# Optimization experiments

Measured on AMD Instinct MI355X. Metric: run time of the kernel, lower is better.

The kernel has to match this reference:

```python
import jax, jax.numpy as jnp
import numpy as np

B, S, IN, OUT, E, K = 4, 4096, 1024, 1024, 8, 2
SCALE = 512.0  # alpha / r = 512 / 1
TEMP = 1.0


def setup_inputs() -> dict:
    key = jax.random.key(0)
    k1, k2, k3, k4 = jax.random.split(key, 4)
    return {
        "x": jax.random.normal(k1, (B, S, IN), dtype=jnp.float32),
        "lora_A": jax.random.normal(k2, (E, 1, IN), dtype=jnp.float32) * 0.02,
        "lora_B": jax.random.normal(k3, (E, OUT, 1), dtype=jnp.float32) * 0.02,
        "gate_w": jax.random.normal(k4, (E, IN), dtype=jnp.float32) * 0.02,
        "gate_b": jnp.zeros((E,), dtype=jnp.float32),
    }


def reference(x, lora_A, lora_B, gate_w, gate_b):
    # segment-level gating: mean over seq, softmax over experts
    seg = x.mean(axis=1)                                    # [B, IN]
    logits = (seg @ gate_w.T + gate_b) / TEMP               # [B, E]
    gate_scores = jax.nn.softmax(logits, axis=-1)           # [B, E]
    topk_scores, topk_idx = jax.lax.top_k(gate_scores, K)   # [B, K] (same for all tokens in segment)

    # dense all-expert LoRA compute (eval mode: dropout is identity)
    h = jnp.einsum('bsi,eri->bser', x, lora_A)              # [B, S, E, r]
    expert_outputs = jnp.einsum('bser,eor->bseo', h, lora_B) * SCALE  # [B, S, E, OUT]

    # gather top-k experts per segment (broadcast over seq) and weighted-sum
    sel = jnp.take_along_axis(expert_outputs, topk_idx[:, None, :, None], axis=2)  # [B, S, K, OUT]
    out = jnp.sum(sel * topk_scores[:, None, :, None], axis=2)  # [B, S, OUT]
    return out
```

## Files before the change

kernel.cpp:

```cpp
#include <hip/hip_runtime.h>

#define SCALE_F 512.0f

#define WS_H     0
#define WS_GPART 131072
#define WS_SELC  147456

__global__ __launch_bounds__(256) void k1_h_gate(
    const float* __restrict__ x, const float* __restrict__ lora_A,
    const float* __restrict__ gate_w, float* __restrict__ h,
    float* __restrict__ gpart)
{
    const int tid  = threadIdx.x;
    const int w    = tid >> 6;
    const int lane = tid & 63;
    const int tok0 = blockIdx.x * 8;

    __shared__ float xbuf[8 * 1024];

    float4 W[4][4];
#pragma unroll
    for (int rr = 0; rr < 4; ++rr) {
        const int row = 4 * w + rr;
        const float* rp = (row < 8) ? (lora_A + row * 1024)
                                    : (gate_w + (row - 8) * 1024);
        const float4* rp4 = (const float4*)rp;
#pragma unroll
        for (int j = 0; j < 4; ++j) W[rr][j] = rp4[lane + 64 * j];
    }

    const float4* src = (const float4*)(x + (size_t)tok0 * 1024);
    float4* dst = (float4*)xbuf;
#pragma unroll
    for (int j = 0; j < 8; ++j) dst[tid + 256 * j] = src[tid + 256 * j];
    __syncthreads();

    float gacc0 = 0.f, gacc1 = 0.f, gacc2 = 0.f, gacc3 = 0.f;

#pragma unroll 2
    for (int t = 0; t < 8; ++t) {
        const float4* xr = (const float4*)(xbuf + t * 1024);
        const float4 xv0 = xr[lane];
        const float4 xv1 = xr[lane + 64];
        const float4 xv2 = xr[lane + 128];
        const float4 xv3 = xr[lane + 192];

        float p[4];
#pragma unroll
        for (int rr = 0; rr < 4; ++rr) {
            const float4 a0 = W[rr][0], a1 = W[rr][1];
            const float4 a2 = W[rr][2], a3 = W[rr][3];
            float s;
            s  = xv0.x * a0.x + xv0.y * a0.y + xv0.z * a0.z + xv0.w * a0.w;
            s += xv1.x * a1.x + xv1.y * a1.y + xv1.z * a1.z + xv1.w * a1.w;
            s += xv2.x * a2.x + xv2.y * a2.y + xv2.z * a2.z + xv2.w * a2.w;
            s += xv3.x * a3.x + xv3.y * a3.y + xv3.z * a3.z + xv3.w * a3.w;
            p[rr] = s;
        }
#pragma unroll
        for (int off = 32; off > 0; off >>= 1) {
            p[0] += __shfl_xor(p[0], off);
            p[1] += __shfl_xor(p[1], off);
            p[2] += __shfl_xor(p[2], off);
            p[3] += __shfl_xor(p[3], off);
        }
        const int tok = tok0 + t;
        if (w < 2) {
            if (lane == 0) {
                float4 hv = make_float4(p[0], p[1], p[2], p[3]);
                *(float4*)(h + (size_t)tok * 8 + w * 4) = hv;
            }
        } else {
            gacc0 += p[0]; gacc1 += p[1]; gacc2 += p[2]; gacc3 += p[3];
        }
    }

    if (w >= 2 && lane == 0) {
        float4 gv = make_float4(gacc0, gacc1, gacc2, gacc3);
        *(float4*)(gpart + (size_t)blockIdx.x * 8 + (w - 2) * 4) = gv;
    }
}

__global__ __launch_bounds__(256) void k2_gate(
    const float* __restrict__ gpart, const float* __restrict__ gate_b,
    int* __restrict__ sel, float* __restrict__ coef)
{
    const int tid  = threadIdx.x;
    const int j    = tid & 7;
    const int pair = tid >> 3;
    const int b    = pair >> 3;
    const int e    = pair & 7;

    __shared__ float s_red[32][8];
    __shared__ float s_logit[32];

    float acc = 0.f;
#pragma unroll 8
    for (int k = 0; k < 64; ++k) {
        acc += gpart[(size_t)(b * 512 + j * 64 + k) * 8 + e];
    }
    s_red[pair][j] = acc;
    __syncthreads();

    if (j == 0) {
        float s = 0.f;
#pragma unroll
        for (int q = 0; q < 8; ++q) s += s_red[pair][q];
        s_logit[pair] = s * (1.0f / 4096.0f) + gate_b[e];
    }
    __syncthreads();

    if (tid < 4) {
        float sc[8];
        float m = -1e30f;
#pragma unroll
        for (int q = 0; q < 8; ++q) { sc[q] = s_logit[tid * 8 + q]; m = fmaxf(m, sc[q]); }
        float sum = 0.f;
#pragma unroll
        for (int q = 0; q < 8; ++q) { sc[q] = __expf(sc[q] - m); sum += sc[q]; }
        const float inv = 1.0f / sum;

        int i0 = 0;
#pragma unroll
        for (int q = 1; q < 8; ++q) if (sc[q] > sc[i0]) i0 = q;
        int i1 = (i0 == 0) ? 1 : 0;
#pragma unroll
        for (int q = 0; q < 8; ++q) if (q != i0 && sc[q] > sc[i1]) i1 = q;

        sel[tid * 2]      = i0;
        sel[tid * 2 + 1]  = i1;
        coef[tid * 2]     = SCALE_F * sc[i0] * inv;
        coef[tid * 2 + 1] = SCALE_F * sc[i1] * inv;
    }
}

__global__ __launch_bounds__(256) void k3_combine(
    const float* __restrict__ h, const int* __restrict__ sel,
    const float* __restrict__ coef, const float* __restrict__ lora_B,
    float* __restrict__ out)
{
    const int tid = threadIdx.x;
    const int blk = blockIdx.x;
    const int b   = blk >> 9;

    const int   i0 = sel[b * 2];
    const int   i1 = sel[b * 2 + 1];
    const float c0 = coef[b * 2];
    const float c1 = coef[b * 2 + 1];

    const float4 b0 = ((const float4*)(lora_B + i0 * 1024))[tid];
    const float4 b1 = ((const float4*)(lora_B + i1 * 1024))[tid];
    const float4 v0 = make_float4(c0 * b0.x, c0 * b0.y, c0 * b0.z, c0 * b0.w);
    const float4 v1 = make_float4(c1 * b1.x, c1 * b1.y, c1 * b1.z, c1 * b1.w);

    const int tok0 = blk * 8;
    float4* out4 = (float4*)out;
#pragma unroll
    for (int t = 0; t < 8; ++t) {
        const int tok = tok0 + t;
        const float h0 = h[tok * 8 + i0];
        const float h1 = h[tok * 8 + i1];
        float4 r;
        r.x = h0 * v0.x + h1 * v1.x;
        r.y = h0 * v0.y + h1 * v1.y;
        r.z = h0 * v0.z + h1 * v1.z;
        r.w = h0 * v0.w + h1 * v1.w;
        out4[(size_t)tok * 256 + tid] = r;
    }
}

extern "C" void kernel_launch(void* const* d_in, const int* in_sizes, int n_in,
                              void* d_out, int out_size, void* d_ws, size_t ws_size,
                              hipStream_t stream) {
    const float* x      = (const float*)d_in[0];
    const float* lora_A = (const float*)d_in[1];
    const float* lora_B = (const float*)d_in[2];
    const float* gate_w = (const float*)d_in[3];
    const float* gate_b = (const float*)d_in[4];
    float* out = (float*)d_out;

    float* ws    = (float*)d_ws;
    float* h     = ws + WS_H;
    float* gpart = ws + WS_GPART;
    int*   sel   = (int*)(ws + WS_SELC);
    float* coef  = ws + WS_SELC + 8;

    k1_h_gate<<<2048, 256, 0, stream>>>(x, lora_A, gate_w, h, gpart);
    k2_gate<<<1, 256, 0, stream>>>(gpart, gate_b, sel, coef);
    k3_combine<<<2048, 256, 0, stream>>>(h, sel, coef, lora_B, out);
}
```

Baseline: 137.9 us.

## Fuse three kernels into one cooperative persistent kernel with grid sync

Replaces the three-launch pipeline (projection plus gate partials, gate softmax/top-k, combine) with a single cooperative kernel. It uses a persistent grid sized by occupancy and a grid-wide barrier between phases, and each block redoes the tiny gate reduction itself. This removes two kernel launches and the serial single-block gate kernel. In exchange it pays the cost of a grid sync, has every block re-read the gate partials, and runs fewer blocks than the original 2048. The three-kernel path is kept as a fallback if the cooperative launch fails.

```diff
diff --git a/kernel.cpp b/kernel.cpp
--- a/kernel.cpp
+++ b/kernel.cpp
@@ -1,10 +1,172 @@
 #include <hip/hip_runtime.h>
+#include <hip/hip_cooperative_groups.h>
+
+namespace cg = cooperative_groups;
 
 #define SCALE_F 512.0f
 
 #define WS_H     0
 #define WS_GPART 131072
 #define WS_SELC  147456
+
+__global__ __launch_bounds__(256) void fused_moe(
+    const float* __restrict__ x, const float* __restrict__ lora_A,
+    const float* __restrict__ lora_B, const float* __restrict__ gate_w,
+    const float* __restrict__ gate_b, float* __restrict__ out,
+    float* __restrict__ h, float* __restrict__ gpart)
+{
+    const int tid  = threadIdx.x;
+    const int w    = tid >> 6;
+    const int lane = tid & 63;
+    const int grid = gridDim.x;
+
+    __shared__ float  xbuf[8 * 1024];
+    __shared__ float4 s_gred[4][2];
+    __shared__ int    s_sel[4][2];
+    __shared__ float  s_coef[4][2];
+
+    float4 W[4][4];
+#pragma unroll
+    for (int rr = 0; rr < 4; ++rr) {
+        const int row = 4 * w + rr;
+        const float* rp = (row < 8) ? (lora_A + row * 1024)
+                                    : (gate_w + (row - 8) * 1024);
+        const float4* rp4 = (const float4*)rp;
+#pragma unroll
+        for (int j = 0; j < 4; ++j) W[rr][j] = rp4[lane + 64 * j];
+    }
+
+    for (int c = blockIdx.x; c < 2048; c += grid) {
+        const int tok0 = c * 8;
+        const float4* src = (const float4*)(x + (size_t)tok0 * 1024);
+        float4* dst = (float4*)xbuf;
+#pragma unroll
+        for (int j = 0; j < 8; ++j) dst[tid + 256 * j] = src[tid + 256 * j];
+        __syncthreads();
+
+        float g0 = 0.f, g1 = 0.f, g2 = 0.f, g3 = 0.f;
+
+#pragma unroll 2
+        for (int t = 0; t < 8; ++t) {
+            const float4* xr = (const float4*)(xbuf + t * 1024);
+            const float4 xv0 = xr[lane];
+            const float4 xv1 = xr[lane + 64];
+            const float4 xv2 = xr[lane + 128];
+            const float4 xv3 = xr[lane + 192];
+
+            float p[4];
+#pragma unroll
+            for (int rr = 0; rr < 4; ++rr) {
+                const float4 a0 = W[rr][0], a1 = W[rr][1];
+                const float4 a2 = W[rr][2], a3 = W[rr][3];
+                float s;
+                s  = xv0.x * a0.x + xv0.y * a0.y + xv0.z * a0.z + xv0.w * a0.w;
+                s += xv1.x * a1.x + xv1.y * a1.y + xv1.z * a1.z + xv1.w * a1.w;
+                s += xv2.x * a2.x + xv2.y * a2.y + xv2.z * a2.z + xv2.w * a2.w;
+                s += xv3.x * a3.x + xv3.y * a3.y + xv3.z * a3.z + xv3.w * a3.w;
+                p[rr] = s;
+            }
+#pragma unroll
+            for (int off = 32; off > 0; off >>= 1) {
+                p[0] += __shfl_xor(p[0], off);
+                p[1] += __shfl_xor(p[1], off);
+                p[2] += __shfl_xor(p[2], off);
+                p[3] += __shfl_xor(p[3], off);
+            }
+            if (w < 2) {
+                if (lane == 0) {
+                    *(float4*)(h + (size_t)(tok0 + t) * 8 + w * 4) =
+                        make_float4(p[0], p[1], p[2], p[3]);
+                }
+            } else {
+                g0 += p[0]; g1 += p[1]; g2 += p[2]; g3 += p[3];
+            }
+        }
+        if (w >= 2 && lane == 0) {
+            *(float4*)(gpart + (size_t)c * 8 + (w - 2) * 4) =
+                make_float4(g0, g1, g2, g3);
+        }
+        __syncthreads();
+    }
+
+    __threadfence();
+    cg::this_grid().sync();
+
+    {
+        const float4* gp4 = (const float4*)(gpart + (size_t)w * 4096);
+        float4 acc = make_float4(0.f, 0.f, 0.f, 0.f);
+#pragma unroll
+        for (int q = 0; q < 16; ++q) {
+            const float4 v = gp4[lane + 64 * q];
+            acc.x += v.x; acc.y += v.y; acc.z += v.z; acc.w += v.w;
+        }
+#pragma unroll
+        for (int off = 2; off <= 32; off <<= 1) {
+            acc.x += __shfl_xor(acc.x, off);
+            acc.y += __shfl_xor(acc.y, off);
+            acc.z += __shfl_xor(acc.z, off);
+            acc.w += __shfl_xor(acc.w, off);
+        }
+        if (lane < 2) s_gred[w][lane] = acc;
+    }
+    __syncthreads();
+
+    if (tid < 4) {
+        const float4 lo = s_gred[tid][0];
+        const float4 hi = s_gred[tid][1];
+        float l[8] = { lo.x, lo.y, lo.z, lo.w, hi.x, hi.y, hi.z, hi.w };
+#pragma unroll
+        for (int e = 0; e < 8; ++e) l[e] = l[e] * (1.0f / 4096.0f) + gate_b[e];
+        float m = l[0];
+#pragma unroll
+        for (int e = 1; e < 8; ++e) m = fmaxf(m, l[e]);
+        float sum = 0.f;
+#pragma unroll
+        for (int e = 0; e < 8; ++e) { l[e] = expf(l[e] - m); sum += l[e]; }
+        const float inv = 1.0f / sum;
+
+        int i0 = 0;
+#pragma unroll
+        for (int e = 1; e < 8; ++e) if (l[e] > l[i0]) i0 = e;
+        int i1 = (i0 == 0) ? 1 : 0;
+#pragma unroll
+        for (int e = 0; e < 8; ++e) if (e != i0 && l[e] > l[i1]) i1 = e;
+
+        s_sel[tid][0]  = i0;
+        s_sel[tid][1]  = i1;
+        s_coef[tid][0] = SCALE_F * l[i0] * inv;
+        s_coef[tid][1] = SCALE_F * l[i1] * inv;
+    }
+    __syncthreads();
+
+    for (int c = blockIdx.x; c < 2048; c += grid) {
+        const int bb = c >> 9;
+        const int   i0 = s_sel[bb][0];
+        const int   i1 = s_sel[bb][1];
+        const float c0 = s_coef[bb][0];
+        const float c1 = s_coef[bb][1];
+
+        const float4 b0 = ((const float4*)(lora_B + i0 * 1024))[tid];
+        const float4 b1 = ((const float4*)(lora_B + i1 * 1024))[tid];
+        const float4 v0 = make_float4(c0 * b0.x, c0 * b0.y, c0 * b0.z, c0 * b0.w);
+        const float4 v1 = make_float4(c1 * b1.x, c1 * b1.y, c1 * b1.z, c1 * b1.w);
+
+        const int tok0 = c * 8;
+        float4* out4 = (float4*)out;
+#pragma unroll 2
+        for (int t = 0; t < 8; ++t) {
+            const int tok = tok0 + t;
+            const float h0 = h[(size_t)tok * 8 + i0];
+            const float h1 = h[(size_t)tok * 8 + i1];
+            float4 r;
+            r.x = h0 * v0.x + h1 * v1.x;
+            r.y = h0 * v0.y + h1 * v1.y;
+            r.z = h0 * v0.z + h1 * v1.z;
+            r.w = h0 * v0.w + h1 * v1.w;
+            out4[(size_t)tok * 256 + tid] = r;
+        }
+    }
+}
 
 __global__ __launch_bounds__(256) void k1_h_gate(
     const float* __restrict__ x, const float* __restrict__ lora_A,
@@ -35,7 +197,7 @@
     for (int j = 0; j < 8; ++j) dst[tid + 256 * j] = src[tid + 256 * j];
     __syncthreads();
 
-    float gacc0 = 0.f, gacc1 = 0.f, gacc2 = 0.f, gacc3 = 0.f;
+    float g0 = 0.f, g1 = 0.f, g2 = 0.f, g3 = 0.f;
 
 #pragma unroll 2
     for (int t = 0; t < 8; ++t) {
@@ -67,17 +229,17 @@
         const int tok = tok0 + t;
         if (w < 2) {
             if (lane == 0) {
-                float4 hv = make_float4(p[0], p[1], p[2], p[3]);
-                *(float4*)(h + (size_t)tok * 8 + w * 4) = hv;
+                *(float4*)(h + (size_t)tok * 8 + w * 4) =
+                    make_float4(p[0], p[1], p[2], p[3]);
             }
         } else {
-            gacc0 += p[0]; gacc1 += p[1]; gacc2 += p[2]; gacc3 += p[3];
+            g0 += p[0]; g1 += p[1]; g2 += p[2]; g3 += p[3];
         }
     }
 
     if (w >= 2 && lane == 0) {
-        float4 gv = make_float4(gacc0, gacc1, gacc2, gacc3);
-        *(float4*)(gpart + (size_t)blockIdx.x * 8 + (w - 2) * 4) = gv;
+        *(float4*)(gpart + (size_t)blockIdx.x * 8 + (w - 2) * 4) =
+            make_float4(g0, g1, g2, g3);
     }
 }
 
@@ -117,7 +279,7 @@
         for (int q = 0; q < 8; ++q) { sc[q] = s_logit[tid * 8 + q]; m = fmaxf(m, sc[q]); }
         float sum = 0.f;
 #pragma unroll
-        for (int q = 0; q < 8; ++q) { sc[q] = __expf(sc[q] - m); sum += sc[q]; }
+        for (int q = 0; q < 8; ++q) { sc[q] = expf(sc[q] - m); sum += sc[q]; }
         const float inv = 1.0f / sum;
 
         int i0 = 0;
@@ -158,8 +320,8 @@
 #pragma unroll
     for (int t = 0; t < 8; ++t) {
         const int tok = tok0 + t;
-        const float h0 = h[tok * 8 + i0];
-        const float h1 = h[tok * 8 + i1];
+        const float h0 = h[(size_t)tok * 8 + i0];
+        const float h1 = h[(size_t)tok * 8 + i1];
         float4 r;
         r.x = h0 * v0.x + h1 * v1.x;
         r.y = h0 * v0.y + h1 * v1.y;
@@ -185,7 +347,32 @@
     int*   sel   = (int*)(ws + WS_SELC);
     float* coef  = ws + WS_SELC + 8;
 
-    k1_h_gate<<<2048, 256, 0, stream>>>(x, lora_A, gate_w, h, gpart);
-    k2_gate<<<1, 256, 0, stream>>>(gpart, gate_b, sel, coef);
-    k3_combine<<<2048, 256, 0, stream>>>(h, sel, coef, lora_B, out);
-}
+    int dev = 0;
+    (void)hipGetDevice(&dev);
+    int numCU = 0;
+    (void)hipDeviceGetAttribute(&numCU, hipDeviceAttributeMultiprocessorCount, dev);
+    int maxBlk = 0;
+    hipError_t occ_err = hipOccupancyMaxActiveBlocksPerMultiprocessor(
+        &maxBlk, fused_moe, 256, 0);
+
+    hipError_t coop_err = hipErrorUnknown;
+    if (occ_err == hipSuccess && numCU > 0 && maxBlk > 0) {
+        int grid = maxBlk * numCU;
+        if (grid > 2048) grid = 2048;
+        if (grid >= 64) {
+            void* kargs[] = {
+                (void*)&x, (void*)&lora_A, (void*)&lora_B, (void*)&gate_w,
+                (void*)&gate_b, (void*)&out, (void*)&h, (void*)&gpart
+            };
+            coop_err = hipLaunchCooperativeKernel((const void*)fused_moe,
+                                                  dim3(grid), dim3(256),
+                                                  kargs, 0, stream);
+        }
+    }
+
+    if (coop_err != hipSuccess) {
+        k1_h_gate<<<2048, 256, 0, stream>>>(x, lora_A, gate_w, h, gpart);
+        k2_gate<<<1, 256, 0, stream>>>(gpart, gate_b, sel, coef);
+        k3_combine<<<2048, 256, 0, stream>>>(h, sel, coef, lora_B, out);
+    }
+}
```

Result: slower. 208.8 us (+51.4%).

## Compute gate from column-summed x instead of per-token gate dot products

Applied to the files above, without the earlier changes.

The gate logits are now computed by first summing x over tokens per block (partial column sums written to workspace), then reducing those in a per-segment k2 kernel and dotting with gate_w once. This removes the per-token gate projection work in k1, so all four waves compute LoRA-A rows split by token halves. It adds an 8 MB partial-sum write plus a serial 512-step reduction in a 4-block k2, and k3 now uses 4096 blocks with 4 tokens each.

```diff
diff --git a/kernel.cpp b/kernel.cpp
--- a/kernel.cpp
+++ b/kernel.cpp
@@ -3,17 +3,18 @@
 #define SCALE_F 512.0f
 
 #define WS_H     0
-#define WS_GPART 131072
-#define WS_SELC  147456
-
-__global__ __launch_bounds__(256) void k1_h_gate(
+#define WS_PCOL  131072
+#define WS_SELC  2228224
+
+__global__ __launch_bounds__(256) void k1_h_colsum(
     const float* __restrict__ x, const float* __restrict__ lora_A,
-    const float* __restrict__ gate_w, float* __restrict__ h,
-    float* __restrict__ gpart)
+    float* __restrict__ h, float* __restrict__ pcol)
 {
     const int tid  = threadIdx.x;
     const int w    = tid >> 6;
     const int lane = tid & 63;
+    const int g    = w & 1;
+    const int th   = w >> 1;
     const int tok0 = blockIdx.x * 8;
 
     __shared__ float xbuf[8 * 1024];
@@ -21,25 +22,27 @@
     float4 W[4][4];
 #pragma unroll
     for (int rr = 0; rr < 4; ++rr) {
-        const int row = 4 * w + rr;
-        const float* rp = (row < 8) ? (lora_A + row * 1024)
-                                    : (gate_w + (row - 8) * 1024);
-        const float4* rp4 = (const float4*)rp;
+        const float4* rp4 = (const float4*)(lora_A + (size_t)(4 * g + rr) * 1024);
 #pragma unroll
         for (int j = 0; j < 4; ++j) W[rr][j] = rp4[lane + 64 * j];
     }
 
     const float4* src = (const float4*)(x + (size_t)tok0 * 1024);
     float4* dst = (float4*)xbuf;
-#pragma unroll
-    for (int j = 0; j < 8; ++j) dst[tid + 256 * j] = src[tid + 256 * j];
+    float4 csum = make_float4(0.f, 0.f, 0.f, 0.f);
+#pragma unroll
+    for (int j = 0; j < 8; ++j) {
+        const float4 v = src[tid + 256 * j];
+        dst[tid + 256 * j] = v;
+        csum.x += v.x; csum.y += v.y; csum.z += v.z; csum.w += v.w;
+    }
+    ((float4*)(pcol + (size_t)blockIdx.x * 1024))[tid] = csum;
     __syncthreads();
 
-    float gacc0 = 0.f, gacc1 = 0.f, gacc2 = 0.f, gacc3 = 0.f;
-
 #pragma unroll 2
-    for (int t = 0; t < 8; ++t) {
-        const float4* xr = (const float4*)(xbuf + t * 1024);
+    for (int t = 0; t < 4; ++t) {
+        const int trow = th * 4 + t;
+        const float4* xr = (const float4*)(xbuf + trow * 1024);
         const float4 xv0 = xr[lane];
         const float4 xv1 = xr[lane + 64];
         const float4 xv2 = xr[lane + 128];
@@ -64,73 +67,85 @@
             p[2] += __shfl_xor(p[2], off);
             p[3] += __shfl_xor(p[3], off);
         }
-        const int tok = tok0 + t;
-        if (w < 2) {
-            if (lane == 0) {
-                float4 hv = make_float4(p[0], p[1], p[2], p[3]);
-                *(float4*)(h + (size_t)tok * 8 + w * 4) = hv;
-            }
-        } else {
-            gacc0 += p[0]; gacc1 += p[1]; gacc2 += p[2]; gacc3 += p[3];
-        }
-    }
-
-    if (w >= 2 && lane == 0) {
-        float4 gv = make_float4(gacc0, gacc1, gacc2, gacc3);
-        *(float4*)(gpart + (size_t)blockIdx.x * 8 + (w - 2) * 4) = gv;
+        if (lane == 0) {
+            *(float4*)(h + (size_t)(tok0 + trow) * 8 + g * 4) =
+                make_float4(p[0], p[1], p[2], p[3]);
+        }
     }
 }
 
 __global__ __launch_bounds__(256) void k2_gate(
-    const float* __restrict__ gpart, const float* __restrict__ gate_b,
-    int* __restrict__ sel, float* __restrict__ coef)
+    const float* __restrict__ pcol, const float* __restrict__ gate_w,
+    const float* __restrict__ gate_b, int* __restrict__ sel,
+    float* __restrict__ coef)
 {
     const int tid  = threadIdx.x;
-    const int j    = tid & 7;
-    const int pair = tid >> 3;
-    const int b    = pair >> 3;
-    const int e    = pair & 7;
-
-    __shared__ float s_red[32][8];
-    __shared__ float s_logit[32];
-
-    float acc = 0.f;
+    const int w    = tid >> 6;
+    const int lane = tid & 63;
+    const int b    = blockIdx.x;
+
+    __shared__ float s_seg[1024];
+    __shared__ float s_logit[8];
+
+    const float4* pc4 = (const float4*)pcol + (size_t)b * 512 * 256;
+    float4 acc = make_float4(0.f, 0.f, 0.f, 0.f);
 #pragma unroll 8
-    for (int k = 0; k < 64; ++k) {
-        acc += gpart[(size_t)(b * 512 + j * 64 + k) * 8 + e];
-    }
-    s_red[pair][j] = acc;
+    for (int p = 0; p < 512; ++p) {
+        const float4 v = pc4[(size_t)p * 256 + tid];
+        acc.x += v.x; acc.y += v.y; acc.z += v.z; acc.w += v.w;
+    }
+    ((float4*)s_seg)[tid] = acc;
     __syncthreads();
 
-    if (j == 0) {
-        float s = 0.f;
-#pragma unroll
-        for (int q = 0; q < 8; ++q) s += s_red[pair][q];
-        s_logit[pair] = s * (1.0f / 4096.0f) + gate_b[e];
+    {
+        const float4* sg4 = (const float4*)s_seg;
+        const float4* w0p = (const float4*)(gate_w + (size_t)(2 * w) * 1024);
+        const float4* w1p = (const float4*)(gate_w + (size_t)(2 * w + 1) * 1024);
+        float p0 = 0.f, p1 = 0.f;
+#pragma unroll
+        for (int j = 0; j < 4; ++j) {
+            const float4 sv = sg4[lane + 64 * j];
+            const float4 w0 = w0p[lane + 64 * j];
+            const float4 w1 = w1p[lane + 64 * j];
+            p0 += sv.x * w0.x + sv.y * w0.y + sv.z * w0.z + sv.w * w0.w;
+            p1 += sv.x * w1.x + sv.y * w1.y + sv.z * w1.z + sv.w * w1.w;
+        }
+#pragma unroll
+        for (int off = 32; off > 0; off >>= 1) {
+            p0 += __shfl_xor(p0, off);
+            p1 += __shfl_xor(p1, off);
+        }
+        if (lane == 0) {
+            s_logit[2 * w]     = p0;
+            s_logit[2 * w + 1] = p1;
+        }
     }
     __syncthreads();
 
-    if (tid < 4) {
-        float sc[8];
-        float m = -1e30f;
-#pragma unroll
-        for (int q = 0; q < 8; ++q) { sc[q] = s_logit[tid * 8 + q]; m = fmaxf(m, sc[q]); }
+    if (tid == 0) {
+        float l[8];
+#pragma unroll
+        for (int e = 0; e < 8; ++e)
+            l[e] = s_logit[e] * (1.0f / 4096.0f) + gate_b[e];
+        float m = l[0];
+#pragma unroll
+        for (int e = 1; e < 8; ++e) m = fmaxf(m, l[e]);
         float sum = 0.f;
 #pragma unroll
-        for (int q = 0; q < 8; ++q) { sc[q] = __expf(sc[q] - m); sum += sc[q]; }
+        for (int e = 0; e < 8; ++e) { l[e] = expf(l[e] - m); sum += l[e]; }
         const float inv = 1.0f / sum;
 
         int i0 = 0;
 #pragma unroll
-        for (int q = 1; q < 8; ++q) if (sc[q] > sc[i0]) i0 = q;
+        for (int e = 1; e < 8; ++e) if (l[e] > l[i0]) i0 = e;
         int i1 = (i0 == 0) ? 1 : 0;
 #pragma unroll
-        for (int q = 0; q < 8; ++q) if (q != i0 && sc[q] > sc[i1]) i1 = q;
-
-        sel[tid * 2]      = i0;
-        sel[tid * 2 + 1]  = i1;
-        coef[tid * 2]     = SCALE_F * sc[i0] * inv;
-        coef[tid * 2 + 1] = SCALE_F * sc[i1] * inv;
+        for (int e = 0; e < 8; ++e) if (e != i0 && l[e] > l[i1]) i1 = e;
+
+        sel[b * 2]      = i0;
+        sel[b * 2 + 1]  = i1;
+        coef[b * 2]     = SCALE_F * l[i0] * inv;
+        coef[b * 2 + 1] = SCALE_F * l[i1] * inv;
     }
 }
 
@@ -141,25 +156,25 @@
 {
     const int tid = threadIdx.x;
     const int blk = blockIdx.x;
-    const int b   = blk >> 9;
+    const int b   = blk >> 10;
 
     const int   i0 = sel[b * 2];
     const int   i1 = sel[b * 2 + 1];
     const float c0 = coef[b * 2];
     const float c1 = coef[b * 2 + 1];
 
-    const float4 b0 = ((const float4*)(lora_B + i0 * 1024))[tid];
-    const float4 b1 = ((const float4*)(lora_B + i1 * 1024))[tid];
+    const float4 b0 = ((const float4*)(lora_B + (size_t)i0 * 1024))[tid];
+    const float4 b1 = ((const float4*)(lora_B + (size_t)i1 * 1024))[tid];
     const float4 v0 = make_float4(c0 * b0.x, c0 * b0.y, c0 * b0.z, c0 * b0.w);
     const float4 v1 = make_float4(c1 * b1.x, c1 * b1.y, c1 * b1.z, c1 * b1.w);
 
-    const int tok0 = blk * 8;
+    const int tok0 = blk * 4;
     float4* out4 = (float4*)out;
 #pragma unroll
-    for (int t = 0; t < 8; ++t) {
+    for (int t = 0; t < 4; ++t) {
         const int tok = tok0 + t;
-        const float h0 = h[tok * 8 + i0];
-        const float h1 = h[tok * 8 + i1];
+        const float h0 = h[(size_t)tok * 8 + i0];
+        const float h1 = h[(size_t)tok * 8 + i1];
         float4 r;
         r.x = h0 * v0.x + h1 * v1.x;
         r.y = h0 * v0.y + h1 * v1.y;
@@ -179,13 +194,13 @@
     const float* gate_b = (const float*)d_in[4];
     float* out = (float*)d_out;
 
-    float* ws    = (float*)d_ws;
-    float* h     = ws + WS_H;
-    float* gpart = ws + WS_GPART;
-    int*   sel   = (int*)(ws + WS_SELC);
-    float* coef  = ws + WS_SELC + 8;
-
-    k1_h_gate<<<2048, 256, 0, stream>>>(x, lora_A, gate_w, h, gpart);
-    k2_gate<<<1, 256, 0, stream>>>(gpart, gate_b, sel, coef);
-    k3_combine<<<2048, 256, 0, stream>>>(h, sel, coef, lora_B, out);
-}
+    float* ws   = (float*)d_ws;
+    float* h    = ws + WS_H;
+    float* pcol = ws + WS_PCOL;
+    int*   sel  = (int*)(ws + WS_SELC);
+    float* coef = ws + WS_SELC + 8;
+
+    k1_h_colsum<<<2048, 256, 0, stream>>>(x, lora_A, h, pcol);
+    k2_gate<<<4, 256, 0, stream>>>(pcol, gate_w, gate_b, sel, coef);
+    k3_combine<<<4096, 256, 0, stream>>>(h, sel, coef, lora_B, out);
+}
```

Result: slower. 154.8 us (+12.2%).
